# Kernel optimization log

Hardware: AMD Instinct MI355X
Metric: run time of the kernel (lower is better)

Reference implementation:

```python
import jax, jax.numpy as jnp
import numpy as np

NF = 128                 # num_filters
C_STATE = NF * 3 // 2    # ODE state channels (output of conv_up_embed_1) = 192
EPS = 1e-5               # InstanceNorm2d eps
N_STEPS = 4              # fixed-step RK4 steps over t in [0, 1]
DT = 1.0 / N_STEPS

nl = jax.nn.softplus     # get_nonlinearity('softplus')


def instance_norm(x):
    # InstanceNorm2d(affine=False): normalize over (H, W) per (N, C)
    m = x.mean(axis=(2, 3), keepdims=True)
    v = x.var(axis=(2, 3), keepdims=True)
    return (x - m) * jax.lax.rsqrt(v + EPS)


def conv2d(x, w, b):
    y = jax.lax.conv_general_dilated(
        x, w, window_strides=(1, 1), padding='SAME',
        dimension_numbers=('NCHW', 'OIHW', 'NCHW'))
    return y + b[None, :, None, None]


def setup_inputs() -> dict:
    key = jax.random.key(0)
    ks = jax.random.split(key, 10)
    B, H, W = 4, 64, 64
    s = 0.05
    return {
        'x':    jax.random.normal(ks[0], (B, NF, H, W), jnp.float32),
        'skip': jax.random.normal(ks[1], (B, NF, 2 * H, 2 * W), jnp.float32),
        # InitialVelocity: 3x3 conv nf -> nf
        'iv_w': jax.random.normal(ks[2], (NF, NF, 3, 3), jnp.float32) * s,
        'iv_b': jax.random.normal(ks[3], (NF,), jnp.float32) * s,
        # conv_up_embed_1: 1x1 conv 3nf -> 3nf//2
        'up_w': jax.random.normal(ks[4], (C_STATE, 3 * NF, 1, 1), jnp.float32) * s,
        'up_b': jax.random.normal(ks[5], (C_STATE,), jnp.float32) * s,
        # ConvSODEFunc convs (second-order: dv/dt = f(z, v))
        'f1_w': jax.random.normal(ks[6], (C_STATE // 2, C_STATE, 3, 3), jnp.float32) * s,
        'f1_b': jax.random.normal(ks[7], (C_STATE // 2,), jnp.float32) * s,
        'f2_w': jax.random.normal(ks[8], (C_STATE // 2, C_STATE // 2, 3, 3), jnp.float32) * s,
        'f2_b': jax.random.normal(ks[9], (C_STATE // 2,), jnp.float32) * s,
    }


def _ode_f(y, f1_w, f1_b, f2_w, f2_b):
    # second-order ODE: state y = [z, v]; dz/dt = v, dv/dt = f(y)
    c = y.shape[1] // 2
    v = y[:, c:]
    u = nl(conv2d(instance_norm(y), f1_w, f1_b))   # [B, C/2, H, W]
    dv = nl(conv2d(instance_norm(u), f2_w, f2_b))  # [B, C/2, H, W]
    return jnp.concatenate([v, dv], axis=1)


def reference(x, skip, iv_w, iv_b, up_w, up_b, f1_w, f1_b, f2_w, f2_b):
    # InitialVelocity (counter == 0): concat learned velocity -> 2*nf channels
    v0 = nl(conv2d(instance_norm(x), iv_w, iv_b))
    y = jnp.concatenate([x, v0], axis=1)                       # [B, 2nf, H, W]
    B, C, H, W = y.shape
    # bilinear upsample x2, align_corners=False (half-pixel centers)
    y = jax.image.resize(y, (B, C, 2 * H, 2 * W), method='bilinear')
    y = jnp.concatenate([y, skip], axis=1)                     # [B, 3nf, 2H, 2W]
    y = nl(conv2d(y, up_w, up_b))                              # [B, 3nf//2, 2H, 2W]
    # ODEBlock: integrate t: 0 -> 1, fixed-step RK4 via lax.scan
    f = lambda s: _ode_f(s, f1_w, f1_b, f2_w, f2_b)

    def step(s, _):
        k1 = f(s)
        k2 = f(s + 0.5 * DT * k1)
        k3 = f(s + 0.5 * DT * k2)
        k4 = f(s + DT * k3)
        s = s + (DT / 6.0) * (k1 + 2.0 * k2 + 2.0 * k3 + k4)
        return s, None

    y, _ = jax.lax.scan(step, y, None, length=N_STEPS)
    return y
```

## Files before the change

kernel.cpp:

```cpp
#include <hip/hip_runtime.h>
#include <math.h>

#define BB 4
#define NF 128
#define CS 192
#define CH 96
#define H1 64
#define W1 64
#define H2 128
#define W2 128
#define P1 (H1*W1)
#define P2 (H2*W2)
#define EPSV 1e-5f
#define DTV 0.25f
#define NSLICE 32
#define SLOTSZ (1536 * NSLICE)

typedef __attribute__((ext_vector_type(8))) short short8;
typedef __attribute__((ext_vector_type(4))) float f32x4;

__device__ __forceinline__ float softplus_f(float x) {
    return fmaxf(x, 0.0f) + __logf(1.0f + __expf(-fabsf(x)));
}
__device__ __forceinline__ unsigned f2bf(float f) {
    unsigned u = __float_as_uint(f);
    return (u + 0x7FFFu + ((u >> 16) & 1u)) >> 16;
}
__device__ __forceinline__ float bf2f(short s) {
    return __uint_as_float(((unsigned)(unsigned short)s) << 16);
}
__device__ __forceinline__ int packbf(float a, float b) {
    return (int)(f2bf(a) | (f2bf(b) << 16));
}

__global__ __launch_bounds__(256) void zero_kernel(float* __restrict__ p, int n) {
    int i = blockIdx.x * 256 + threadIdx.x;
    if (i < n) p[i] = 0.f;
}

__global__ __launch_bounds__(256) void meanvar_raw_kernel(const float* __restrict__ x,
                                                          float* __restrict__ mv, int HW) {
    int bc = blockIdx.x;
    const float* p = x + (size_t)bc * HW;
    float s = 0.f, s2 = 0.f;
    for (int i = threadIdx.x; i < HW; i += 256) {
        float v = p[i];
        s += v; s2 += v * v;
    }
    __shared__ float sh[512];
    sh[threadIdx.x] = s; sh[256 + threadIdx.x] = s2;
    __syncthreads();
    for (int o = 128; o > 0; o >>= 1) {
        if (threadIdx.x < o) {
            sh[threadIdx.x] += sh[threadIdx.x + o];
            sh[256 + threadIdx.x] += sh[256 + threadIdx.x + o];
        }
        __syncthreads();
    }
    if (threadIdx.x == 0) {
        mv[2 * bc]     = sh[0];
        mv[2 * bc + 1] = sh[256];
    }
}

__global__ __launch_bounds__(256) void repack_w_kernel(const float* __restrict__ w,
                                                       short* __restrict__ wq,
                                                       int Cout, int Cin) {
    int idx = blockIdx.x * 256 + threadIdx.x;
    int total = Cout * Cin * 9;
    if (idx >= total) return;
    int tap = idx % 9;
    int t = idx / 9;
    int ci = t % Cin, co = t / Cin;
    int COGl = Cout >> 4;
    int cog = co >> 4, lx = co & 15;
    int it = ci >> 5, q = (ci >> 3) & 3, e = ci & 7;
    size_t o = (((size_t)(it * 9 + tap) * COGl + cog) * 64 + q * 16 + lx) * 8 + e;
    wq[o] = (short)f2bf(w[idx]);
}

__global__ __launch_bounds__(256) void repack_w1_kernel(const float* __restrict__ w,
                                                        short* __restrict__ wq,
                                                        int Cout, int Cin) {
    int idx = blockIdx.x * 256 + threadIdx.x;
    if (idx >= Cout * Cin) return;
    int ci = idx % Cin, co = idx / Cin;
    int COGl = Cout >> 4;
    int cog = co >> 4, lx = co & 15;
    int it = ci >> 5, q = (ci >> 3) & 3, e = ci & 7;
    size_t o = (((size_t)it * COGl + cog) * 64 + q * 16 + lx) * 8 + e;
    wq[o] = (short)f2bf(w[idx]);
}

__global__ __launch_bounds__(256) void xcvt_kernel(const float* __restrict__ x,
                                                   short* __restrict__ xbf) {
    __shared__ int buf[64 * 68];
    const int tid = threadIdx.x;
    const int px = tid & 63, jj = tid >> 6;
    const int px0 = blockIdx.x * 64;
    const int b = blockIdx.y;
#pragma unroll
    for (int ji = 0; ji < 16; ji++) {
        int j = jj + 4 * ji;
        int c = 2 * j;
        float a = x[((size_t)(b * NF + c)) * P1 + px0 + px];
        float d = x[((size_t)(b * NF + c + 1)) * P1 + px0 + px];
        buf[px * 68 + j] = packbf(a, d);
    }
    __syncthreads();
#pragma unroll
    for (int k = 0; k < 4; k++) {
        int idx = tid + 256 * k;
        int p2 = idx >> 4, w4 = idx & 15;
        int4 v = *(const int4*)&buf[p2 * 68 + w4 * 4];
        *(int4*)(xbf + ((size_t)b * P1 + px0 + p2) * NF + w4 * 8) = v;
    }
}

template<int CIN, int NCG, bool OUTBF, bool SUMS>
__global__ __launch_bounds__(256) void conv3x3_mfma(
    const short* __restrict__ in, const float* __restrict__ mvsums,
    const short* __restrict__ wq, const float* __restrict__ bias,
    float* __restrict__ outf, short* __restrict__ outbf, float* __restrict__ osum,
    int CoutT, int H, int W, int outC, int outCoff, int coblk)
{
    constexpr int ROWS = CIN + 8;
    constexpr int STGI = 180 * ROWS / 2;
    constexpr int SMEMI = (OUTBF && 128 * 52 > STGI) ? 128 * 52 : STGI;
    constexpr int NCGH = NCG / 2;
    __shared__ int smem[SMEMI];
    short* xt = (short*)smem;
    __shared__ float mvm[CIN], mvr[CIN];
    __shared__ float shs[2 * CH];
    const int tid = threadIdx.x;
    const int w4 = tid >> 6, lane = tid & 63;
    const int wy = w4 & 1, wc = w4 >> 1;
    const int lx = lane & 15, q = lane >> 4;
    const int x0 = blockIdx.x * 16, y0 = blockIdx.y * 8;
    const int b = blockIdx.z / coblk;
    const int co_base = (blockIdx.z % coblk) * (NCG * 16);
    const int slice = (blockIdx.x + (blockIdx.y << 3)) & (NSLICE - 1);
    const int HWp = H * W;
    const short* inb = in + (size_t)b * HWp * CIN;

    const float invHW = 1.0f / (float)HWp;
    for (int c = tid; c < CIN; c += 256) {
        float s = 0.f, s2 = 0.f;
#pragma unroll
        for (int sl = 0; sl < NSLICE; sl++) {
            s  += mvsums[(size_t)sl * 1536 + (b * CIN + c) * 2];
            s2 += mvsums[(size_t)sl * 1536 + (b * CIN + c) * 2 + 1];
        }
        float m  = s * invHW;
        float var = fmaxf(s2 * invHW - m * m, 0.f);
        mvm[c] = m;
        mvr[c] = rsqrtf(var + EPSV);
    }
    if (SUMS) for (int c = tid; c < 2 * CH; c += 256) shs[c] = 0.f;
    __syncthreads();

    constexpr int PARTS = CIN / 8;
    constexpr int TOT = 180 * PARTS;
    constexpr int NJ = (TOT + 255) / 256;
#pragma unroll
    for (int k = 0; k < NJ; k++) {
        int j = tid + 256 * k;
        if (j < TOT) {
            int px = j / PARTS, part = j - px * PARTS;
            int yy = px / 18, xx = px - yy * 18;
            int gy = y0 + yy - 1, gx = x0 + xx - 1;
            int4 wv = make_int4(0, 0, 0, 0);
            if (gy >= 0 && gy < H && gx >= 0 && gx < W) {
                int cb = part * 8;
                short8 v = *(const short8*)(inb + (size_t)(gy * W + gx) * CIN + cb);
                float4 m0 = *(const float4*)&mvm[cb];
                float4 m1 = *(const float4*)&mvm[cb + 4];
                float4 r0 = *(const float4*)&mvr[cb];
                float4 r1 = *(const float4*)&mvr[cb + 4];
                wv.x = packbf((bf2f(v[0]) - m0.x) * r0.x, (bf2f(v[1]) - m0.y) * r0.y);
                wv.y = packbf((bf2f(v[2]) - m0.z) * r0.z, (bf2f(v[3]) - m0.w) * r0.w);
                wv.z = packbf((bf2f(v[4]) - m1.x) * r1.x, (bf2f(v[5]) - m1.y) * r1.y);
                wv.w = packbf((bf2f(v[6]) - m1.z) * r1.z, (bf2f(v[7]) - m1.w) * r1.w);
            }
            *(int4*)(&xt[px * ROWS + part * 8]) = wv;
        }
    }
    __syncthreads();

    f32x4 acc[4][NCGH];
#pragma unroll
    for (int rr = 0; rr < 4; rr++)
#pragma unroll
        for (int cg = 0; cg < NCGH; cg++) acc[rr][cg] = (f32x4)(0.f);

    constexpr int NIT = CIN / 32;
    constexpr int NC = 9 * NIT;
    const int COGl = CoutT >> 4;
    const short* wbase = wq + ((size_t)((co_base >> 4) + wc * NCGH) * 64 + lane) * 8;
    const size_t wstep = (size_t)COGl * 512;

    auto ldw = [&](int c, short8* dst) {
#pragma unroll
        for (int cg = 0; cg < NCGH; cg++)
            dst[cg] = *(const short8*)(wbase + (size_t)c * wstep + (size_t)cg * 512);
    };
    auto ldb = [&](int c, short8* dst) {
        const int it = c / 9, tap = c - 9 * (c / 9);
        const int dy = tap / 3, dx = tap - 3 * (tap / 3);
#pragma unroll
        for (int rr = 0; rr < 4; rr++)
            dst[rr] = *(const short8*)(
                &xt[((wy * 4 + rr + dy) * 18 + lx + dx) * ROWS + it * 32 + q * 8]);
    };
    auto fma = [&](const short8* a, const short8* bfr) {
#pragma unroll
        for (int rr = 0; rr < 4; rr++)
#pragma unroll
            for (int cg = 0; cg < NCGH; cg++)
                acc[rr][cg] = __builtin_amdgcn_mfma_f32_16x16x32_bf16(
                    a[cg], bfr[rr], acc[rr][cg], 0, 0, 0);
    };

    short8 aA[NCGH], aB[NCGH], aC[NCGH];
    short8 bA[4], bB[4], bC[4];
    ldw(0, aA);
    ldw(1, aB);
    ldb(0, bA);
#pragma unroll
    for (int c = 0; c < NC; c += 3) {
        if (c + 2 < NC) ldw(c + 2, aC);
        if (c + 1 < NC) ldb(c + 1, bB);
        fma(aA, bA);
        if (c + 3 < NC) ldw(c + 3, aA);
        if (c + 2 < NC) ldb(c + 2, bC);
        if (c + 1 < NC) fma(aB, bB);
        if (c + 4 < NC) ldw(c + 4, aB);
        if (c + 3 < NC) ldb(c + 3, bA);
        if (c + 2 < NC) fma(aC, bC);
    }

    if (OUTBF) __syncthreads();

    float s1l[NCGH][4], s2l[NCGH][4];
    if (SUMS) {
#pragma unroll
        for (int cg = 0; cg < NCGH; cg++)
#pragma unroll
            for (int r = 0; r < 4; r++) { s1l[cg][r] = 0.f; s2l[cg][r] = 0.f; }
    }
#pragma unroll
    for (int rr = 0; rr < 4; rr++) {
        int y = y0 + wy * 4 + rr;
#pragma unroll
        for (int cg = 0; cg < NCGH; cg++) {
            float v[4];
#pragma unroll
            for (int r = 0; r < 4; r++) {
                int co = wc * (NCGH * 16) + cg * 16 + q * 4 + r;
                v[r] = softplus_f(acc[rr][cg][r] + bias[co_base + co]);
                if (SUMS) { s1l[cg][r] += v[r]; s2l[cg][r] += v[r] * v[r]; }
            }
            if (OUTBF) {
                int pl = (wy * 4 + rr) * 16 + lx;
                smem[pl * 52 + wc * (NCGH * 8) + cg * 8 + q * 2]     = packbf(v[0], v[1]);
                smem[pl * 52 + wc * (NCGH * 8) + cg * 8 + q * 2 + 1] = packbf(v[2], v[3]);
            } else {
                float* ob = outf + ((size_t)b * outC + outCoff + co_base) * HWp
                            + y * W + x0 + lx;
#pragma unroll
                for (int r = 0; r < 4; r++)
                    ob[(size_t)(wc * (NCGH * 16) + cg * 16 + q * 4 + r) * HWp] = v[r];
            }
        }
    }
    if (OUTBF) {
        __syncthreads();
#pragma unroll
        for (int k = 0; k < 6; k++) {
            int idx = tid + 256 * k;
            int pl2 = idx / 12, w4i = idx % 12;
            int4 v = *(const int4*)&smem[pl2 * 52 + w4i * 4];
            int pix = (y0 + (pl2 >> 4)) * W + x0 + (pl2 & 15);
            *(int4*)(outbf + ((size_t)b * HWp + pix) * 96 + w4i * 8) = v;
        }
    }
    if (SUMS) {
#pragma unroll
        for (int cg = 0; cg < NCGH; cg++)
#pragma unroll
            for (int r = 0; r < 4; r++) {
                float a1 = s1l[cg][r], a2 = s2l[cg][r];
#pragma unroll
                for (int mask = 1; mask < 16; mask <<= 1) {
                    a1 += __shfl_xor(a1, mask);
                    a2 += __shfl_xor(a2, mask);
                }
                if (lx == 0) {
                    int co = wc * (NCGH * 16) + cg * 16 + q * 4 + r;
                    atomicAdd(&shs[2 * co], a1);
                    atomicAdd(&shs[2 * co + 1], a2);
                }
            }
        __syncthreads();
        for (int c = tid; c < 2 * NCG * 16; c += 256)
            atomicAdd(&osum[(size_t)slice * 1536 + (size_t)b * 2 * NCG * 16 + c], shs[c]);
    }
}

__global__ __launch_bounds__(256) void upsample_kernel(
    const float* __restrict__ x, const float* __restrict__ v0,
    const float* __restrict__ skip, short* __restrict__ ycat)
{
    __shared__ int buf[64 * 98];
    const int tid = threadIdx.x;
    const int px = tid & 63, jj = tid >> 6;
    const int ox0 = (blockIdx.x & 3) * 32;
    const int oy0 = (blockIdx.x >> 2) * 2;
    const int b = blockIdx.y;
    const int ox = ox0 + (px & 31), oy = oy0 + (px >> 5);
    const int pxg = oy * W2 + ox;
    int my = oy >> 1, mx = ox >> 1;
    int iy0 = (oy & 1) ? my : my - 1;
    float wy0 = (oy & 1) ? 0.75f : 0.25f;
    int ix0 = (ox & 1) ? mx : mx - 1;
    float wx0 = (ox & 1) ? 0.75f : 0.25f;
    int iy1 = min(iy0 + 1, H1 - 1); iy0 = max(iy0, 0);
    int ix1 = min(ix0 + 1, W1 - 1); ix0 = max(ix0, 0);
    float wy1 = 1.f - wy0, wx1 = 1.f - wx0;
    float w00 = wy0 * wx0, w01 = wy0 * wx1, w10 = wy1 * wx0, w11 = wy1 * wx1;
    int o00 = iy0 * W1 + ix0, o01 = iy0 * W1 + ix1;
    int o10 = iy1 * W1 + ix0, o11 = iy1 * W1 + ix1;

#pragma unroll
    for (int half = 0; half < 2; half++) {
        if (half == 1) __syncthreads();
#pragma unroll 4
        for (int ji = 0; ji < 24; ji++) {
            int j = jj + 4 * ji + half * 96;
            int c = 2 * j;
            float a, d;
            if (c < 256) {
                const float* s0 = (c < 128) ? x + ((size_t)(b * NF + c)) * P1
                                            : v0 + ((size_t)(b * NF + c - 128)) * P1;
                const float* s1 = s0 + P1;
                a = w00 * s0[o00] + w01 * s0[o01] + w10 * s0[o10] + w11 * s0[o11];
                d = w00 * s1[o00] + w01 * s1[o01] + w10 * s1[o10] + w11 * s1[o11];
            } else {
                const float* sk = skip + ((size_t)(b * NF + c - 256)) * P2 + pxg;
                a = sk[0]; d = sk[P2];
            }
            buf[px * 98 + (j - half * 96)] = packbf(a, d);
        }
        __syncthreads();
#pragma unroll
        for (int k = 0; k < 6; k++) {
            int idx = tid + 256 * k;
            int p2 = idx / 24, w4 = idx % 24;
            int4 v = *(const int4*)&buf[p2 * 98 + w4 * 4];
            int pix = (oy0 + (p2 >> 5)) * W2 + ox0 + (p2 & 31);
            *(int4*)(ycat + ((size_t)b * P2 + pix) * 384 + half * 192 + w4 * 8) = v;
        }
    }
}

__global__ __launch_bounds__(256, 4) void conv1x1_mfma(
    const short* __restrict__ ycat, const short* __restrict__ wq,
    const float* __restrict__ bias, float* __restrict__ out,
    short* __restrict__ sbf, float* __restrict__ osum)
{
    __shared__ int smem[64 * 100];
    short* xs = (short*)smem;
    const int tid = threadIdx.x;
    const int wave = tid >> 6, lane = tid & 63;
    const int lx = lane & 15, q = lane >> 4;
    const int p0 = blockIdx.x * 64;
    const int b = blockIdx.y;
    const int slice = blockIdx.x & (NSLICE - 1);

    f32x4 acc[3][4];
#pragma unroll
    for (int cg = 0; cg < 3; cg++)
#pragma unroll
        for (int pg = 0; pg < 4; pg++) acc[cg][pg] = (f32x4)(0.f);

    const short* wbase = wq + ((size_t)(wave * 3) * 64 + lane) * 8;
    auto ldw = [&](int it, short8* dst) {
#pragma unroll
        for (int cg = 0; cg < 3; cg++)
            dst[cg] = *(const short8*)(wbase + (size_t)(it * 12 + cg) * 512);
    };
    auto mbody = [&](int itl, const short8* a) {
        short8 bfr[4];
#pragma unroll
        for (int pg = 0; pg < 4; pg++)
            bfr[pg] = *(const short8*)(&xs[(pg * 16 + lx) * 200 + itl * 32 + q * 8]);
#pragma unroll
        for (int pg = 0; pg < 4; pg++)
#pragma unroll
            for (int cg = 0; cg < 3; cg++)
                acc[cg][pg] = __builtin_amdgcn_mfma_f32_16x16x32_bf16(
                    a[cg], bfr[pg], acc[cg][pg], 0, 0, 0);
    };

    const short* yb = ycat + ((size_t)b * P2 + p0) * 384;
#pragma unroll
    for (int half = 0; half < 2; half++) {
        if (half == 1) __syncthreads();
#pragma unroll
        for (int k = 0; k < 6; k++) {
            int j = tid + 256 * k;
            int spx = j / 24, spart = j - spx * 24;
            short8 v = *(const short8*)(yb + (size_t)spx * 384 + half * 192 + spart * 8);
            *(short8*)(&xs[spx * 200 + spart * 8]) = v;
        }
        __syncthreads();

        short8 aA[3], aB[3], aC[3];
        ldw(half * 6 + 0, aA);
        ldw(half * 6 + 1, aB);
#pragma unroll
        for (int c = 0; c < 6; c += 3) {
            ldw(half * 6 + c + 2, aC);
            mbody(c, aA);
            if (c + 3 < 6) ldw(half * 6 + c + 3, aA);
            mbody(c + 1, aB);
            if (c + 4 < 6) ldw(half * 6 + c + 4, aB);
            mbody(c + 2, aC);
        }
    }
    __syncthreads();

    float s1a[3][4], s2a[3][4];
#pragma unroll
    for (int cg = 0; cg < 3; cg++)
#pragma unroll
        for (int r = 0; r < 4; r++) { s1a[cg][r] = 0.f; s2a[cg][r] = 0.f; }
#pragma unroll
    for (int cg = 0; cg < 3; cg++) {
        int co0 = wave * 48 + cg * 16 + q * 4;
#pragma unroll
        for (int pg = 0; pg < 4; pg++) {
            int pl = pg * 16 + lx;
            float v[4];
#pragma unroll
            for (int r = 0; r < 4; r++) {
                v[r] = softplus_f(acc[cg][pg][r] + bias[co0 + r]);
                out[((size_t)(b * CS + co0 + r)) * P2 + p0 + pl] = v[r];
                s1a[cg][r] += v[r]; s2a[cg][r] += v[r] * v[r];
            }
            smem[pl * 100 + (co0 >> 1)]     = packbf(v[0], v[1]);
            smem[pl * 100 + (co0 >> 1) + 1] = packbf(v[2], v[3]);
        }
    }
    __syncthreads();
#pragma unroll
    for (int k = 0; k < 6; k++) {
        int idx = tid + 256 * k;
        int p2 = idx / 24, w4 = idx % 24;
        int4 v = *(const int4*)&smem[p2 * 100 + w4 * 4];
        *(int4*)(sbf + ((size_t)b * P2 + p0 + p2) * 192 + w4 * 8) = v;
    }
#pragma unroll
    for (int cg = 0; cg < 3; cg++)
#pragma unroll
        for (int r = 0; r < 4; r++) {
            float a1 = s1a[cg][r], a2 = s2a[cg][r];
#pragma unroll
            for (int mask = 1; mask < 16; mask <<= 1) {
                a1 += __shfl_xor(a1, mask);
                a2 += __shfl_xor(a2, mask);
            }
            if (lx == 0) {
                int co = wave * 48 + cg * 16 + q * 4 + r;
                atomicAdd(&osum[(size_t)slice * 1536 + ((size_t)b * CS + co) * 2], a1);
                atomicAdd(&osum[(size_t)slice * 1536 + ((size_t)b * CS + co) * 2 + 1], a2);
            }
        }
}

__global__ __launch_bounds__(256) void combine_kernel(
    const float* __restrict__ S, const float* __restrict__ Gx,
    const float* __restrict__ Gp, short* __restrict__ T, float* __restrict__ osum,
    float ca1, float ca2, float cb)
{
    __shared__ int buf[64 * 100];
    const int tid = threadIdx.x;
    const int px = tid & 63, jj = tid >> 6;
    const int px0 = blockIdx.x * 64;
    const int b = blockIdx.y;
    const int pxg = px0 + px;
    const int slice = blockIdx.x & (NSLICE - 1);
#pragma unroll 3
    for (int ji = 0; ji < 12; ji++) {
        int j = jj + 4 * ji;
        int c = 2 * j;
        size_t ia = ((size_t)(b * CS + c)) * P2 + pxg;
        size_t ib = ia + (size_t)CH * P2;
        size_t ig = ((size_t)(b * CH + c)) * P2 + pxg;
        float sa0 = S[ia], sa1 = S[ia + P2];
        float sb0 = S[ib], sb1 = S[ib + P2];
        float gx0 = Gx[ig], gx1 = Gx[ig + P2];
        float gp0 = Gp[ig], gp1 = Gp[ig + P2];
        buf[px * 100 + j]      = packbf(sa0 + ca1 * sb0 + ca2 * gx0,
                                        sa1 + ca1 * sb1 + ca2 * gx1);
        buf[px * 100 + 48 + j] = packbf(sb0 + cb * gp0, sb1 + cb * gp1);
    }
    __syncthreads();
#pragma unroll
    for (int k = 0; k < 6; k++) {
        int idx = tid + 256 * k;
        int p2 = idx / 24, w4 = idx % 24;
        int4 v = *(const int4*)&buf[p2 * 100 + w4 * 4];
        *(int4*)(T + ((size_t)b * P2 + px0 + p2) * 192 + w4 * 8) = v;
    }
    if (tid < 192) {
        int jj2 = tid >> 1, s = tid & 1;
        float s1lo = 0.f, s2lo = 0.f, s1hi = 0.f, s2hi = 0.f;
#pragma unroll 8
        for (int p = s; p < 64; p += 2) {
            int v = buf[p * 100 + jj2];
            float lo = bf2f((short)v), hi = bf2f((short)(v >> 16));
            s1lo += lo; s2lo += lo * lo; s1hi += hi; s2hi += hi * hi;
        }
        s1lo += __shfl_xor(s1lo, 1); s2lo += __shfl_xor(s2lo, 1);
        s1hi += __shfl_xor(s1hi, 1); s2hi += __shfl_xor(s2hi, 1);
        if (s == 0) {
            int c = 2 * jj2;
            float* dst = &osum[(size_t)slice * 1536 + ((size_t)b * CS + c) * 2];
            atomicAdd(dst, s1lo);
            atomicAdd(dst + 1, s2lo);
            atomicAdd(dst + 2, s1hi);
            atomicAdd(dst + 3, s2hi);
        }
    }
}

template<bool SBF>
__global__ __launch_bounds__(256) void final_kernel(
    float* __restrict__ S, const float* __restrict__ G1, const float* __restrict__ G2,
    const float* __restrict__ G3, const float* __restrict__ G4,
    short* __restrict__ sbf, float* __restrict__ osum)
{
    __shared__ int buf[SBF ? 64 * 100 : 4];
    const int tid = threadIdx.x;
    const int px = tid & 63, jj = tid >> 6;
    const int px0 = blockIdx.x * 64;
    const int b = blockIdx.y;
    const int pxg = px0 + px;
    const int slice = blockIdx.x & (NSLICE - 1);
    const float cA = DTV * DTV / 6.0f, cB = DTV / 6.0f;
#pragma unroll 3
    for (int ji = 0; ji < 12; ji++) {
        int j = jj + 4 * ji;
        int c = 2 * j;
        size_t ia = ((size_t)(b * CS + c)) * P2 + pxg;
        size_t ib = ia + (size_t)CH * P2;
        size_t ig = ((size_t)(b * CH + c)) * P2 + pxg;
        float sa0 = S[ia], sa1 = S[ia + P2];
        float sb0 = S[ib], sb1 = S[ib + P2];
        float g10 = G1[ig], g11 = G1[ig + P2];
        float g20 = G2[ig], g21 = G2[ig + P2];
        float g30 = G3[ig], g31 = G3[ig + P2];
        float g40 = G4[ig], g41 = G4[ig + P2];
        float na0 = sa0 + DTV * sb0 + cA * (g10 + g20 + g30);
        float na1 = sa1 + DTV * sb1 + cA * (g11 + g21 + g31);
        float nb0 = sb0 + cB * (g10 + 2.f * g20 + 2.f * g30 + g40);
        float nb1 = sb1 + cB * (g11 + 2.f * g21 + 2.f * g31 + g41);
        S[ia] = na0; S[ia + P2] = na1;
        S[ib] = nb0; S[ib + P2] = nb1;
        if (SBF) {
            buf[px * 100 + j]      = packbf(na0, na1);
            buf[px * 100 + 48 + j] = packbf(nb0, nb1);
        }
    }
    if (SBF) {
        __syncthreads();
#pragma unroll
        for (int k = 0; k < 6; k++) {
            int idx = tid + 256 * k;
            int p2 = idx / 24, w4 = idx % 24;
            int4 v = *(const int4*)&buf[p2 * 100 + w4 * 4];
            *(int4*)(sbf + ((size_t)b * P2 + px0 + p2) * 192 + w4 * 8) = v;
        }
        if (tid < 192) {
            int jj2 = tid >> 1, s = tid & 1;
            float s1lo = 0.f, s2lo = 0.f, s1hi = 0.f, s2hi = 0.f;
#pragma unroll 8
            for (int p = s; p < 64; p += 2) {
                int v = buf[p * 100 + jj2];
                float lo = bf2f((short)v), hi = bf2f((short)(v >> 16));
                s1lo += lo; s2lo += lo * lo; s1hi += hi; s2hi += hi * hi;
            }
            s1lo += __shfl_xor(s1lo, 1); s2lo += __shfl_xor(s2lo, 1);
            s1hi += __shfl_xor(s1hi, 1); s2hi += __shfl_xor(s2hi, 1);
            if (s == 0) {
                int c = 2 * jj2;
                float* dst = &osum[(size_t)slice * 1536 + ((size_t)b * CS + c) * 2];
                atomicAdd(dst, s1lo);
                atomicAdd(dst + 1, s2lo);
                atomicAdd(dst + 2, s1hi);
                atomicAdd(dst + 3, s2hi);
            }
        }
    }
}

extern "C" void kernel_launch(void* const* d_in, const int* in_sizes, int n_in,
                              void* d_out, int out_size, void* d_ws, size_t ws_size,
                              hipStream_t stream) {
    (void)in_sizes; (void)n_in; (void)out_size; (void)ws_size;
    const float* x    = (const float*)d_in[0];
    const float* skip = (const float*)d_in[1];
    const float* iv_w = (const float*)d_in[2];
    const float* iv_b = (const float*)d_in[3];
    const float* up_w = (const float*)d_in[4];
    const float* up_b = (const float*)d_in[5];
    const float* f1_w = (const float*)d_in[6];
    const float* f1_b = (const float*)d_in[7];
    const float* f2_w = (const float*)d_in[8];
    const float* f2_b = (const float*)d_in[9];

    float* S = (float*)d_out;
    float* ws = (float*)d_ws;
    const size_t NGf = (size_t)BB * CH * P2;
    float* G1 = ws;
    float* G2 = G1 + NGf;
    float* G3 = G2 + NGf;
    float* G4 = G3 + NGf;
    short* T   = (short*)(G4 + NGf);
    short* U   = T + (size_t)BB * P2 * CS;
    short* SBF = U + (size_t)BB * P2 * CH;
    float* MVS = (float*)(SBF + (size_t)BB * P2 * CS);
    short* IVQ = (short*)(MVS + (size_t)34 * SLOTSZ);
    short* F1Q = IVQ + (size_t)9 * NF * NF;
    short* F2Q = F1Q + (size_t)9 * CH * CS;
    short* UPQ = F2Q + (size_t)9 * CH * CH;
    short* YCAT = (short*)G1;
    float* V0   = G3;
    short* XBF  = (short*)G4;

    auto slot = [&](int i) { return MVS + (size_t)i * SLOTSZ; };

    zero_kernel<<<(34 * SLOTSZ + 255) / 256, 256, 0, stream>>>(MVS, 34 * SLOTSZ);
    repack_w_kernel<<<(NF * NF * 9 + 255) / 256, 256, 0, stream>>>(iv_w, IVQ, NF, NF);
    repack_w_kernel<<<(CH * CS * 9 + 255) / 256, 256, 0, stream>>>(f1_w, F1Q, CH, CS);
    repack_w_kernel<<<(CH * CH * 9 + 255) / 256, 256, 0, stream>>>(f2_w, F2Q, CH, CH);
    repack_w1_kernel<<<(CS * 384 + 255) / 256, 256, 0, stream>>>(up_w, UPQ, CS, 384);

    meanvar_raw_kernel<<<BB * NF, 256, 0, stream>>>(x, slot(0), P1);
    xcvt_kernel<<<dim3(P1 / 64, BB), 256, 0, stream>>>(x, XBF);
    conv3x3_mfma<128, 4, false, false><<<dim3(W1 / 16, H1 / 8, BB * 2), 256, 0, stream>>>(
        XBF, slot(0), IVQ, iv_b, V0, nullptr, nullptr, NF, H1, W1, NF, 0, 2);
    upsample_kernel<<<dim3(P2 / 64, BB), 256, 0, stream>>>(x, V0, skip, YCAT);
    conv1x1_mfma<<<dim3(P2 / 64, BB), 256, 0, stream>>>(YCAT, UPQ, up_b, S, SBF, slot(1));

    const float h = DTV;
    float* G[4] = {G1, G2, G3, G4};
    int sc = 2;
    float* yslot = slot(1);
    const dim3 egrd(P2 / 64, BB);

    for (int step = 0; step < 4; step++) {
        for (int sub = 0; sub < 4; sub++) {
            const short* Ybf = (sub == 0) ? SBF : T;
            float* uslot = slot(sc++);
            conv3x3_mfma<192, 6, true, true><<<dim3(W2 / 16, H2 / 8, BB), 256, 0, stream>>>(
                Ybf, yslot, F1Q, f1_b, nullptr, U, uslot, CH, H2, W2, CH, 0, 1);
            conv3x3_mfma<96, 6, false, false><<<dim3(W2 / 16, H2 / 8, BB), 256, 0, stream>>>(
                U, uslot, F2Q, f2_b, G[sub], nullptr, nullptr, CH, H2, W2, CH, 0, 1);
            if (sub < 3) {
                float ca1, ca2, cb;
                const float *Gx, *Gp;
                if (sub == 0)      { ca1 = h/2; ca2 = 0.f;     Gx = G1; Gp = G1; cb = h/2; }
                else if (sub == 1) { ca1 = h/2; ca2 = h*h/4;   Gx = G1; Gp = G2; cb = h/2; }
                else               { ca1 = h;   ca2 = h*h/2;   Gx = G2; Gp = G3; cb = h;   }
                float* tslot = slot(sc++);
                combine_kernel<<<egrd, 256, 0, stream>>>(S, Gx, Gp, T, tslot, ca1, ca2, cb);
                yslot = tslot;
            }
        }
        if (step < 3) {
            float* sslot = slot(sc++);
            final_kernel<true><<<egrd, 256, 0, stream>>>(S, G1, G2, G3, G4, SBF, sslot);
            yslot = sslot;
        } else {
            final_kernel<false><<<egrd, 256, 0, stream>>>(S, G1, G2, G3, G4, SBF, nullptr);
        }
    }
}
```

Baseline: 1.432 ms.

## Fuse RK4 stage-combine into second conv epilogue, removing combine kernel

The separate combine_kernel that built the next RK4 stage input T (bf16, NHWC) and its instance-norm partial sums is folded into the epilogue of the f2 conv. The conv now reads S and the prior G directly, uses its freshly computed dv values in registers instead of re-reading G from global memory, writes T through shared memory, and accumulates stats per tile. This removes 12 kernel launches and one full read of G per stage, at the cost of a larger shared-memory footprint (128*100 ints) and more epilogue work in the conv, which may lower occupancy.

```diff
diff --git a/kernel.cpp b/kernel.cpp
--- a/kernel.cpp
+++ b/kernel.cpp
@@ -117,16 +117,20 @@
     }
 }
 
-template<int CIN, int NCG, bool OUTBF, bool SUMS>
+template<int CIN, int NCG, bool OUTBF, bool FUSET, bool SUMS>
 __global__ __launch_bounds__(256) void conv3x3_mfma(
     const short* __restrict__ in, const float* __restrict__ mvsums,
     const short* __restrict__ wq, const float* __restrict__ bias,
     float* __restrict__ outf, short* __restrict__ outbf, float* __restrict__ osum,
-    int CoutT, int H, int W, int outC, int outCoff, int coblk)
+    int CoutT, int H, int W, int outC, int outCoff, int coblk,
+    const float* __restrict__ Sg, const float* __restrict__ Gxg,
+    short* __restrict__ Tout, float* __restrict__ tosum,
+    float ca1, float ca2, float cb)
 {
     constexpr int ROWS = CIN + 8;
     constexpr int STGI = 180 * ROWS / 2;
-    constexpr int SMEMI = (OUTBF && 128 * 52 > STGI) ? 128 * 52 : STGI;
+    constexpr int SMEMI = FUSET ? (STGI > 128 * 100 ? STGI : 128 * 100)
+                                : ((OUTBF && 128 * 52 > STGI) ? 128 * 52 : STGI);
     constexpr int NCGH = NCG / 2;
     __shared__ int smem[SMEMI];
     short* xt = (short*)smem;
@@ -171,12 +175,12 @@
             int gy = y0 + yy - 1, gx = x0 + xx - 1;
             int4 wv = make_int4(0, 0, 0, 0);
             if (gy >= 0 && gy < H && gx >= 0 && gx < W) {
-                int cb = part * 8;
-                short8 v = *(const short8*)(inb + (size_t)(gy * W + gx) * CIN + cb);
-                float4 m0 = *(const float4*)&mvm[cb];
-                float4 m1 = *(const float4*)&mvm[cb + 4];
-                float4 r0 = *(const float4*)&mvr[cb];
-                float4 r1 = *(const float4*)&mvr[cb + 4];
+                int cb2 = part * 8;
+                short8 v = *(const short8*)(inb + (size_t)(gy * W + gx) * CIN + cb2);
+                float4 m0 = *(const float4*)&mvm[cb2];
+                float4 m1 = *(const float4*)&mvm[cb2 + 4];
+                float4 r0 = *(const float4*)&mvr[cb2];
+                float4 r1 = *(const float4*)&mvr[cb2 + 4];
                 wv.x = packbf((bf2f(v[0]) - m0.x) * r0.x, (bf2f(v[1]) - m0.y) * r0.y);
                 wv.y = packbf((bf2f(v[2]) - m0.z) * r0.z, (bf2f(v[3]) - m0.w) * r0.w);
                 wv.z = packbf((bf2f(v[4]) - m1.x) * r1.x, (bf2f(v[5]) - m1.y) * r1.y);
@@ -239,7 +243,9 @@
         if (c + 2 < NC) fma(aC, bC);
     }
 
-    if (OUTBF) __syncthreads();
+    if (OUTBF || FUSET) __syncthreads();
+
+    const bool doT = FUSET && (Tout != nullptr);
 
     float s1l[NCGH][4], s2l[NCGH][4];
     if (SUMS) {
@@ -270,6 +276,27 @@
 #pragma unroll
                 for (int r = 0; r < 4; r++)
                     ob[(size_t)(wc * (NCGH * 16) + cg * 16 + q * 4 + r) * HWp] = v[r];
+                if (doT) {
+                    int co0 = wc * (NCGH * 16) + cg * 16 + q * 4;
+                    const float* Sa = Sg + ((size_t)b * CS + co0) * HWp + y * W + x0 + lx;
+                    const float* Sb = Sa + (size_t)CH * HWp;
+                    const float* Gx = Gxg ? (Gxg + ((size_t)b * CH + co0) * HWp
+                                             + y * W + x0 + lx) : nullptr;
+                    float ta[4], tb[4];
+#pragma unroll
+                    for (int r = 0; r < 4; r++) {
+                        float sa = Sa[(size_t)r * HWp];
+                        float sb = Sb[(size_t)r * HWp];
+                        float gx = Gx ? Gx[(size_t)r * HWp] : 0.f;
+                        ta[r] = sa + ca1 * sb + ca2 * gx;
+                        tb[r] = sb + cb * v[r];
+                    }
+                    int pl = (wy * 4 + rr) * 16 + lx;
+                    smem[pl * 100 + (co0 >> 1)]          = packbf(ta[0], ta[1]);
+                    smem[pl * 100 + (co0 >> 1) + 1]      = packbf(ta[2], ta[3]);
+                    smem[pl * 100 + 48 + (co0 >> 1)]     = packbf(tb[0], tb[1]);
+                    smem[pl * 100 + 48 + (co0 >> 1) + 1] = packbf(tb[2], tb[3]);
+                }
             }
         }
     }
@@ -282,6 +309,37 @@
             int4 v = *(const int4*)&smem[pl2 * 52 + w4i * 4];
             int pix = (y0 + (pl2 >> 4)) * W + x0 + (pl2 & 15);
             *(int4*)(outbf + ((size_t)b * HWp + pix) * 96 + w4i * 8) = v;
+        }
+    }
+    if (doT) {
+        __syncthreads();
+#pragma unroll
+        for (int k = 0; k < 12; k++) {
+            int idx = tid + 256 * k;
+            int pl2 = idx / 24, w4i = idx % 24;
+            int4 v = *(const int4*)&smem[pl2 * 100 + w4i * 4];
+            int pix = (y0 + (pl2 >> 4)) * W + x0 + (pl2 & 15);
+            *(int4*)(Tout + ((size_t)b * HWp + pix) * 192 + w4i * 8) = v;
+        }
+        if (tid < 192) {
+            int jj2 = tid >> 1, s = tid & 1;
+            float s1lo = 0.f, s2lo = 0.f, s1hi = 0.f, s2hi = 0.f;
+#pragma unroll 8
+            for (int p = s; p < 128; p += 2) {
+                int v = smem[p * 100 + jj2];
+                float lo = bf2f((short)v), hi = bf2f((short)(v >> 16));
+                s1lo += lo; s2lo += lo * lo; s1hi += hi; s2hi += hi * hi;
+            }
+            s1lo += __shfl_xor(s1lo, 1); s2lo += __shfl_xor(s2lo, 1);
+            s1hi += __shfl_xor(s1hi, 1); s2hi += __shfl_xor(s2hi, 1);
+            if (s == 0) {
+                int c = 2 * jj2;
+                float* dst = &tosum[(size_t)slice * 1536 + ((size_t)b * CS + c) * 2];
+                atomicAdd(dst, s1lo);
+                atomicAdd(dst + 1, s2lo);
+                atomicAdd(dst + 2, s1hi);
+                atomicAdd(dst + 3, s2hi);
+            }
         }
     }
     if (SUMS) {
@@ -476,63 +534,6 @@
                 atomicAdd(&osum[(size_t)slice * 1536 + ((size_t)b * CS + co) * 2 + 1], a2);
             }
         }
-}
-
-__global__ __launch_bounds__(256) void combine_kernel(
-    const float* __restrict__ S, const float* __restrict__ Gx,
-    const float* __restrict__ Gp, short* __restrict__ T, float* __restrict__ osum,
-    float ca1, float ca2, float cb)
-{
-    __shared__ int buf[64 * 100];
-    const int tid = threadIdx.x;
-    const int px = tid & 63, jj = tid >> 6;
-    const int px0 = blockIdx.x * 64;
-    const int b = blockIdx.y;
-    const int pxg = px0 + px;
-    const int slice = blockIdx.x & (NSLICE - 1);
-#pragma unroll 3
-    for (int ji = 0; ji < 12; ji++) {
-        int j = jj + 4 * ji;
-        int c = 2 * j;
-        size_t ia = ((size_t)(b * CS + c)) * P2 + pxg;
-        size_t ib = ia + (size_t)CH * P2;
-        size_t ig = ((size_t)(b * CH + c)) * P2 + pxg;
-        float sa0 = S[ia], sa1 = S[ia + P2];
-        float sb0 = S[ib], sb1 = S[ib + P2];
-        float gx0 = Gx[ig], gx1 = Gx[ig + P2];
-        float gp0 = Gp[ig], gp1 = Gp[ig + P2];
-        buf[px * 100 + j]      = packbf(sa0 + ca1 * sb0 + ca2 * gx0,
-                                        sa1 + ca1 * sb1 + ca2 * gx1);
-        buf[px * 100 + 48 + j] = packbf(sb0 + cb * gp0, sb1 + cb * gp1);
-    }
-    __syncthreads();
-#pragma unroll
-    for (int k = 0; k < 6; k++) {
-        int idx = tid + 256 * k;
-        int p2 = idx / 24, w4 = idx % 24;
-        int4 v = *(const int4*)&buf[p2 * 100 + w4 * 4];
-        *(int4*)(T + ((size_t)b * P2 + px0 + p2) * 192 + w4 * 8) = v;
-    }
-    if (tid < 192) {
-        int jj2 = tid >> 1, s = tid & 1;
-        float s1lo = 0.f, s2lo = 0.f, s1hi = 0.f, s2hi = 0.f;
-#pragma unroll 8
-        for (int p = s; p < 64; p += 2) {
-            int v = buf[p * 100 + jj2];
-            float lo = bf2f((short)v), hi = bf2f((short)(v >> 16));
-            s1lo += lo; s2lo += lo * lo; s1hi += hi; s2hi += hi * hi;
-        }
-        s1lo += __shfl_xor(s1lo, 1); s2lo += __shfl_xor(s2lo, 1);
-        s1hi += __shfl_xor(s1hi, 1); s2hi += __shfl_xor(s2hi, 1);
-        if (s == 0) {
-            int c = 2 * jj2;
-            float* dst = &osum[(size_t)slice * 1536 + ((size_t)b * CS + c) * 2];
-            atomicAdd(dst, s1lo);
-            atomicAdd(dst + 1, s2lo);
-            atomicAdd(dst + 2, s1hi);
-            atomicAdd(dst + 3, s2hi);
-        }
-    }
 }
 
 template<bool SBF>
@@ -649,8 +650,9 @@
 
     meanvar_raw_kernel<<<BB * NF, 256, 0, stream>>>(x, slot(0), P1);
     xcvt_kernel<<<dim3(P1 / 64, BB), 256, 0, stream>>>(x, XBF);
-    conv3x3_mfma<128, 4, false, false><<<dim3(W1 / 16, H1 / 8, BB * 2), 256, 0, stream>>>(
-        XBF, slot(0), IVQ, iv_b, V0, nullptr, nullptr, NF, H1, W1, NF, 0, 2);
+    conv3x3_mfma<128, 4, false, false, false><<<dim3(W1 / 16, H1 / 8, BB * 2), 256, 0, stream>>>(
+        XBF, slot(0), IVQ, iv_b, V0, nullptr, nullptr, NF, H1, W1, NF, 0, 2,
+        nullptr, nullptr, nullptr, nullptr, 0.f, 0.f, 0.f);
     upsample_kernel<<<dim3(P2 / 64, BB), 256, 0, stream>>>(x, V0, skip, YCAT);
     conv1x1_mfma<<<dim3(P2 / 64, BB), 256, 0, stream>>>(YCAT, UPQ, up_b, S, SBF, slot(1));
 
@@ -658,27 +660,32 @@
     float* G[4] = {G1, G2, G3, G4};
     int sc = 2;
     float* yslot = slot(1);
-    const dim3 egrd(P2 / 64, BB);
 
     for (int step = 0; step < 4; step++) {
         for (int sub = 0; sub < 4; sub++) {
             const short* Ybf = (sub == 0) ? SBF : T;
             float* uslot = slot(sc++);
-            conv3x3_mfma<192, 6, true, true><<<dim3(W2 / 16, H2 / 8, BB), 256, 0, stream>>>(
-                Ybf, yslot, F1Q, f1_b, nullptr, U, uslot, CH, H2, W2, CH, 0, 1);
-            conv3x3_mfma<96, 6, false, false><<<dim3(W2 / 16, H2 / 8, BB), 256, 0, stream>>>(
-                U, uslot, F2Q, f2_b, G[sub], nullptr, nullptr, CH, H2, W2, CH, 0, 1);
+            conv3x3_mfma<192, 6, true, false, true><<<dim3(W2 / 16, H2 / 8, BB), 256, 0, stream>>>(
+                Ybf, yslot, F1Q, f1_b, nullptr, U, uslot, CH, H2, W2, CH, 0, 1,
+                nullptr, nullptr, nullptr, nullptr, 0.f, 0.f, 0.f);
             if (sub < 3) {
                 float ca1, ca2, cb;
-                const float *Gx, *Gp;
-                if (sub == 0)      { ca1 = h/2; ca2 = 0.f;     Gx = G1; Gp = G1; cb = h/2; }
-                else if (sub == 1) { ca1 = h/2; ca2 = h*h/4;   Gx = G1; Gp = G2; cb = h/2; }
-                else               { ca1 = h;   ca2 = h*h/2;   Gx = G2; Gp = G3; cb = h;   }
+                const float* Gx;
+                if (sub == 0)      { ca1 = h/2; ca2 = 0.f;     Gx = nullptr; cb = h/2; }
+                else if (sub == 1) { ca1 = h/2; ca2 = h*h/4;   Gx = G1;      cb = h/2; }
+                else               { ca1 = h;   ca2 = h*h/2;   Gx = G2;      cb = h;   }
                 float* tslot = slot(sc++);
-                combine_kernel<<<egrd, 256, 0, stream>>>(S, Gx, Gp, T, tslot, ca1, ca2, cb);
+                conv3x3_mfma<96, 6, false, true, false><<<dim3(W2 / 16, H2 / 8, BB), 256, 0, stream>>>(
+                    U, uslot, F2Q, f2_b, G[sub], nullptr, nullptr, CH, H2, W2, CH, 0, 1,
+                    S, Gx, T, tslot, ca1, ca2, cb);
                 yslot = tslot;
-            }
-        }
+            } else {
+                conv3x3_mfma<96, 6, false, true, false><<<dim3(W2 / 16, H2 / 8, BB), 256, 0, stream>>>(
+                    U, uslot, F2Q, f2_b, G[sub], nullptr, nullptr, CH, H2, W2, CH, 0, 1,
+                    nullptr, nullptr, nullptr, nullptr, 0.f, 0.f, 0.f);
+            }
+        }
+        const dim3 egrd(P2 / 64, BB);
         if (step < 3) {
             float* sslot = slot(sc++);
             final_kernel<true><<<egrd, 256, 0, stream>>>(S, G1, G2, G3, G4, SBF, sslot);
```

Measured after the change: 1.464 ms. +2.2%, slower.
